# Kernel tuning notes

Hardware: AMD Instinct MI355X
Metric: run time of the kernel (lower is better)

The kernel has to match this reference:

```python
import jax, jax.numpy as jnp
import numpy as np

N_SIGMA = 2
N_CLASS = 8
FG_WEIGHT = jnp.array([10., 10., 10., 40., 80., 100., 60., 20.], dtype=jnp.float32)
W_INST, W_VAR, W_SEED = 1.0, 10.0, 1.0
MIN_PIXELS = 128


def lovasz_hinge_flat(logits, labels):
    # logits, labels: [P] flat; labels in {0,1}
    signs = 2.0 * labels - 1.0
    errors = 1.0 - logits * signs
    order = jnp.argsort(-errors)  # descending
    errors_sorted = errors[order]
    gt_sorted = labels[order]
    gts = gt_sorted.sum()
    inter = gts - jnp.cumsum(gt_sorted)
    union = gts + jnp.cumsum(1.0 - gt_sorted)
    jac = 1.0 - inter / union
    grad = jnp.concatenate([jac[:1], jac[1:] - jac[:-1]])
    return jnp.dot(jax.nn.relu(errors_sorted), jax.lax.stop_gradient(grad))


def setup_inputs() -> dict:
    key = jax.random.key(0)
    k1, k2, k3, k4 = jax.random.split(key, 4)
    B, H, W, N = 2, 512, 1024, 8
    prediction = jax.random.normal(k1, (B, 12, H, W), dtype=jnp.float32)
    bbox = jax.random.randint(k2, (B, 9, H, W), 0, 2, dtype=jnp.int32)
    masks = jax.random.randint(k3, (B, N, H, W), 0, 2, dtype=jnp.int32)
    cls_ids = jax.random.randint(k4, (B, N), 0, 8, dtype=jnp.int32)
    return {"prediction": prediction, "bbox": bbox, "masks": masks, "cls_ids": cls_ids}


def _forward(prediction, bbox, masks, cls_ids):
    B, C, H, W = prediction.shape
    N = masks.shape[1]
    sg = jax.lax.stop_gradient
    # coordinate map: full 2048/1024 linspace sliced to [:W]/[:H], as in the buffer
    xm = jnp.linspace(0.0, 2.0, 2048, dtype=prediction.dtype)[:W]
    ym = jnp.linspace(0.0, 1.0, 1024, dtype=prediction.dtype)[:H]
    xym = jnp.stack([jnp.broadcast_to(xm[None, :], (H, W)),
                     jnp.broadcast_to(ym[:, None], (H, W))], axis=0)  # [2,H,W]

    spatial_emb = jnp.tanh(prediction[:, 0:2]) + xym[None]            # [B,2,H,W]
    sigma = prediction[:, 2:2 + N_SIGMA]                               # [B,2,H,W]
    seed = jax.nn.sigmoid(prediction[:, 2 + N_SIGMA:2 + N_SIGMA + N_CLASS])  # [B,8,H,W]

    # background seed loss: sum over cls 1..8 of seed[cls-1]^2 where bbox[cls]==0
    bg = bbox[:, 1:9] == 0                                             # [B,8,H,W]
    seed_bg = jnp.sum(jnp.where(bg, seed * seed, 0.0), axis=(1, 2, 3))  # [B]

    m = (masks > 0).astype(prediction.dtype)                           # [B,N,H,W]
    cnt = m.sum(axis=(2, 3))                                           # [B,N]
    valid = (cnt >= MIN_PIXELS).astype(prediction.dtype)               # [B,N]
    cnt_safe = jnp.maximum(cnt, 1.0)

    # per-instance masked means (to_center=False -> center from spatial_emb)
    center = jnp.einsum('bnhw,bchw->bnc', m, spatial_emb) / cnt_safe[..., None]  # [B,N,2]
    s_mean = jnp.einsum('bnhw,bchw->bnc', m, sigma) / cnt_safe[..., None]        # [B,N,2]

    # var loss: mean over [n_sigma, P] of (sigma_in - s.detach())^2
    diff2 = (sigma[:, None] - sg(s_mean)[..., None, None]) ** 2        # [B,N,2,H,W]
    var_inst = jnp.einsum('bnchw,bnhw->bn', diff2, m) / (N_SIGMA * cnt_safe)

    s_exp = jnp.exp(s_mean * 10.0)                                     # [B,N,2]
    d2 = (spatial_emb[:, None] - center[..., None, None]) ** 2         # [B,N,2,H,W]
    dist = jnp.exp(-jnp.einsum('bnchw,bnc->bnhw', d2, s_exp))          # [B,N,H,W]

    # lovasz hinge per instance on dist*2-1 vs mask
    logits = (dist * 2.0 - 1.0).reshape(B * N, H * W)
    labels = m.reshape(B * N, H * W)
    lov = jax.vmap(lovasz_hinge_flat)(logits, labels).reshape(B, N)    # [B,N]

    # foreground seed loss
    seed_cls = jnp.take_along_axis(seed, cls_ids[..., None, None].astype(jnp.int32), axis=1)  # [B,N,H,W]
    fw = FG_WEIGHT[cls_ids]                                            # [B,N]
    seed_fg = fw * jnp.einsum('bnhw,bnhw->bn', m, (seed_cls - sg(dist)) ** 2)

    obj = valid.sum(axis=1)                                            # [B]
    obj_safe = jnp.maximum(obj, 1.0)
    inst_l = jnp.sum(lov * valid, axis=1) / obj_safe
    var_l = jnp.sum(var_inst * valid, axis=1) / obj_safe
    seed_l = (seed_bg + jnp.sum(seed_fg * valid, axis=1)) / (H * W)
    loss = jnp.mean(W_INST * inst_l + W_VAR * var_l + W_SEED * seed_l)
    return loss


def reference(prediction, bbox, masks, cls_ids):
    return _forward(prediction, bbox, masks, cls_ids)
```

## Files before the change

### kernel.cpp

```cpp
#include <hip/hip_runtime.h>
#include <cstdint>
#include <cstddef>

#define HW 524288
#define HW4 131072
#define NBIN 1024


__device__ __forceinline__ float wred(float v) {
#pragma unroll
  for (int o = 32; o > 0; o >>= 1) v += __shfl_xor(v, o, 64);
  return v;
}

__device__ __forceinline__ float fsig(float x) {
  return __builtin_amdgcn_rcpf(1.f + __expf(-x));
}
__device__ __forceinline__ float ftanh(float x) {
  return 1.f - 2.f * __builtin_amdgcn_rcpf(__expf(2.f * x) + 1.f);
}

__global__ __launch_bounds__(256) void pass1(
    const float* __restrict__ pred, const int* __restrict__ masks,
    double* __restrict__ acc)
{
  const int b = blockIdx.y;
  const int tid = threadIdx.x;
  const float4* pb4 = (const float4*)(pred + (size_t)b * 12 * HW);
  const int4*   mk4 = (const int4*)(masks + (size_t)b * 8 * HW);

  float c[8] = {0}, cx[8] = {0}, cy[8] = {0}, sx[8] = {0}, sy[8] = {0},
        sxx[8] = {0}, syy[8] = {0};

#pragma unroll
  for (int k = 0; k < 2; k++) {
    const int g = blockIdx.x * 512 + k * 256 + tid;
    int idx = g << 2;
    int h = idx >> 10, w = idx & 1023;
    float4 p0 = pb4[g];
    float4 p1 = pb4[HW4 + g];
    float4 s0 = pb4[2 * HW4 + g];
    float4 s1 = pb4[3 * HW4 + g];
    int4 mv[8];
#pragma unroll
    for (int n = 0; n < 8; n++) mv[n] = mk4[n * HW4 + g];

    float p0v[4] = {p0.x, p0.y, p0.z, p0.w}, p1v[4] = {p1.x, p1.y, p1.z, p1.w};
    float s0v[4] = {s0.x, s0.y, s0.z, s0.w}, s1v[4] = {s1.x, s1.y, s1.z, s1.w};
    float exv[4], eyv[4];
#pragma unroll
    for (int j = 0; j < 4; j++) {
      exv[j] = ftanh(p0v[j]) + (float)((w + j) * (2.0 / 2047.0));
      eyv[j] = ftanh(p1v[j]) + (float)(h * (1.0 / 1023.0));
    }
#pragma unroll
    for (int n = 0; n < 8; n++) {
      int mvv[4] = {mv[n].x, mv[n].y, mv[n].z, mv[n].w};
#pragma unroll
      for (int j = 0; j < 4; j++) {
        float mf = (mvv[j] > 0) ? 1.f : 0.f;
        c[n] += mf; cx[n] += mf * exv[j]; cy[n] += mf * eyv[j];
        sx[n] += mf * s0v[j]; sy[n] += mf * s1v[j];
        sxx[n] += mf * s0v[j] * s0v[j]; syy[n] += mf * s1v[j] * s1v[j];
      }
    }
  }

  __shared__ float red[4][56];
  int lane = tid & 63, wid = tid >> 6;
#pragma unroll
  for (int n = 0; n < 8; n++) {
    float r0 = wred(c[n]),  r1 = wred(cx[n]), r2 = wred(cy[n]),
          r3 = wred(sx[n]), r4 = wred(sy[n]), r5 = wred(sxx[n]),
          r6 = wred(syy[n]);
    if (lane == 0) {
      red[wid][n * 7 + 0] = r0; red[wid][n * 7 + 1] = r1;
      red[wid][n * 7 + 2] = r2; red[wid][n * 7 + 3] = r3;
      red[wid][n * 7 + 4] = r4; red[wid][n * 7 + 5] = r5;
      red[wid][n * 7 + 6] = r6;
    }
  }
  __syncthreads();
  if (tid < 56) {
    float s = red[0][tid] + red[1][tid] + red[2][tid] + red[3][tid];
    int n = tid / 7, q = tid % 7;
    atomicAdd(&acc[((size_t)b * 8 + n) * 8 + q], (double)s);
  }
}

__global__ __launch_bounds__(1024) void pass3(
    const float* __restrict__ pred, const int* __restrict__ bbox,
    const int* __restrict__ masks, const int* __restrict__ cls_ids,
    double* __restrict__ acc, double* __restrict__ seedbg,
    unsigned long long* __restrict__ ghist)
{
  const int seg = blockIdx.y;
  const int b = seg >> 3, n = seg & 7;
  const int tid = threadIdx.x;
  __shared__ unsigned hist[NBIN];
  __shared__ float redf[16][2];
  for (int j = tid; j < NBIN; j += 1024) hist[j] = 0;

  const double* a = acc + seg * 8;
  double cntd = a[0];
  double cs = cntd < 1.0 ? 1.0 : cntd;
  float cxv = (float)(a[1] / cs), cyv = (float)(a[2] / cs);
  float sex = __expf((float)(a[3] / cs) * 10.f);
  float sey = __expf((float)(a[4] / cs) * 10.f);
  int cls = cls_ids[b * 8 + n];
  const float4* pb4 = (const float4*)(pred + (size_t)b * 12 * HW);
  const float4* sp4 = pb4 + (size_t)(4 + cls) * HW4;
  const float4* sb4 = pb4 + (size_t)(4 + n) * HW4;
  const int4*   mp4 = (const int4*)(masks + (size_t)seg * HW);
  const int4*   bb4 = (const int4*)(bbox + (size_t)b * 9 * HW) + (1 + n) * HW4;
  __syncthreads();

  float sf = 0.f, sbg = 0.f;
  int gbase = blockIdx.x * 4096;
#pragma unroll
  for (int i = 0; i < 4; i++) {
    int g = gbase + i * 1024 + tid;
    int idx = g << 2;
    int h = idx >> 10, w = idx & 1023;
    float4 p0 = pb4[g];
    float4 p1 = pb4[HW4 + g];
    int4 mv = mp4[g];
    float4 sv = sp4[g];
    float4 sb = sb4[g];
    int4 bv = bb4[g];
    float p0v[4] = {p0.x, p0.y, p0.z, p0.w}, p1v[4] = {p1.x, p1.y, p1.z, p1.w};
    float svv[4] = {sv.x, sv.y, sv.z, sv.w}, sbv[4] = {sb.x, sb.y, sb.z, sb.w};
    int mvv[4] = {mv.x, mv.y, mv.z, mv.w}, bvv[4] = {bv.x, bv.y, bv.z, bv.w};
#pragma unroll
    for (int j = 0; j < 4; j++) {
      int m = (mvv[j] > 0) ? 1 : 0;
      float ex = ftanh(p0v[j]) + (float)((w + j) * (2.0 / 2047.0));
      float ey = ftanh(p1v[j]) + (float)(h * (1.0 / 1023.0));
      float dx = ex - cxv, dy = ey - cyv;
      float d = __expf(-(dx * dx * sex + dy * dy * sey));
      float df = fsig(svv[j]) - d;
      sf += m ? df * df : 0.f;
      float sgb = fsig(sbv[j]);
      sbg += (bvv[j] == 0) ? sgb * sgb : 0.f;
      float e = m ? 2.f - 2.f * d : 2.f * d;
      int k = (int)(e * 512.f); k = k > (NBIN - 1) ? (NBIN - 1) : k;
      atomicAdd(&hist[k], m ? 65536u : 1u);
    }
  }
  __syncthreads();

  unsigned long long* gh = ghist + (size_t)seg * NBIN;
  for (int j = tid; j < NBIN; j += 1024) {
    unsigned v = hist[j];
    if (v)
      atomicAdd(&gh[j], (unsigned long long)(v & 0xffffu) |
                        ((unsigned long long)(v >> 16) << 32));
  }

  float r0 = wred(sf), r1 = wred(sbg);
  int lane = tid & 63, wid = tid >> 6;
  if (lane == 0) { redf[wid][0] = r0; redf[wid][1] = r1; }
  __syncthreads();
  if (tid == 0) {
    float t = 0.f;
    for (int w2 = 0; w2 < 16; w2++) t += redf[w2][0];
    atomicAdd(&acc[seg * 8 + 7], (double)t);
  } else if (tid == 64) {
    float t = 0.f;
    for (int w2 = 0; w2 < 16; w2++) t += redf[w2][1];
    atomicAdd(&seedbg[b], (double)t);
  }
}

__global__ __launch_bounds__(256) void pass4(
    const unsigned long long* __restrict__ ghist, const double* __restrict__ acc,
    const double* __restrict__ seedbg, const int* __restrict__ cls_ids,
    float* __restrict__ lov, unsigned* __restrict__ ctr,
    float* __restrict__ out)
{
  const int seg = blockIdx.x;
  const int tid = threadIdx.x;
  const int lane = tid & 63, wid = tid >> 6;
  __shared__ __align__(16) unsigned lh[NBIN * 2];
  __shared__ unsigned wc[4], wp[4];
  __shared__ double sred[4];

  const uint4* gh4 = (const uint4*)(ghist + (size_t)seg * NBIN);
#pragma unroll
  for (int i = 0; i < 2; i++)
    ((uint4*)lh)[i * 256 + tid] = gh4[i * 256 + tid];
  __syncthreads();

  double G = acc[seg * 8 + 0];

  unsigned cntT = 0, posT = 0;
#pragma unroll
  for (int i = 0; i < 4; i++) {
    int kk = (NBIN - 1) - tid * 4 - i;
    unsigned h0 = lh[2 * kk], h1 = lh[2 * kk + 1];
    cntT += h0 + h1; posT += h1;
  }
  unsigned ic = cntT, ip = posT;
  for (int o = 1; o < 64; o <<= 1) {
    unsigned yc = __shfl_up(ic, o, 64), yp = __shfl_up(ip, o, 64);
    if (lane >= o) { ic += yc; ip += yp; }
  }
  if (lane == 63) { wc[wid] = ic; wp[wid] = ip; }
  __syncthreads();
  unsigned oc = 0, op = 0;
  for (int w2 = 0; w2 < wid; w2++) { oc += wc[w2]; op += wp[w2]; }
  unsigned p = oc + ic - cntT, C = op + ip - posT;

  double S = 0.0;
#pragma unroll
  for (int i = 0; i < 4; i++) {
    int kk = (NBIN - 1) - tid * 4 - i;
    unsigned n1 = lh[2 * kk + 1], n0 = lh[2 * kk];
    double ec = (kk + 0.5) * (1.0 / 512.0);
    if (n1) {
      S += (double)n1 * ec / (G + (double)(p - C));
      p += n1; C += n1;
    }
    if (n0) {
      double rem = G - (double)C;
      if (rem > 0.0) {
        double aa = G + (double)(p - C);
        S += ec * rem * (1.0 / aa - 1.0 / (aa + (double)n0));
      }
      p += n0;
    }
  }
#pragma unroll
  for (int o = 32; o > 0; o >>= 1) S += __shfl_xor(S, o, 64);
  if (lane == 0) sred[wid] = S;
  __syncthreads();

  if (tid == 0) {
    double St = sred[0] + sred[1] + sred[2] + sred[3];
    atomicExch(&lov[seg], (float)St);
    __threadfence();
    unsigned old = atomicAdd(ctr, 1u);
    if (old == 15u) {
      __threadfence();
      const float FG[8] = {10.f, 10.f, 10.f, 40.f, 80.f, 100.f, 60.f, 20.f};
      double total = 0.0;
      for (int b = 0; b < 2; b++) {
        double obj = 0, inst = 0, varl = 0, sfg = 0;
        for (int n = 0; n < 8; n++) {
          int s = b * 8 + n;
          const double* a = acc + s * 8;
          double cnt = a[0];
          double cs = cnt < 1.0 ? 1.0 : cnt;
          double smx = a[3] / cs, smy = a[4] / cs;
          double var = ((a[5] - cnt * smx * smx) + (a[6] - cnt * smy * smy)) /
                       (2.0 * cs);
          double v = (cnt >= 128.0) ? 1.0 : 0.0;
          double lv = (double)atomicAdd(&lov[s], 0.0f);
          obj += v;
          inst += lv * v;
          varl += var * v;
          sfg += (double)FG[cls_ids[s]] * a[7] * v;
        }
        double objs = obj < 1.0 ? 1.0 : obj;
        double seedl = (seedbg[b] + sfg) / (double)HW;
        total += inst / objs + 10.0 * (varl / objs) + seedl;
      }
      out[0] = (float)(0.5 * total);
    }
  }
}

extern "C" void kernel_launch(void* const* d_in, const int* in_sizes, int n_in,
                              void* d_out, int out_size, void* d_ws, size_t ws_size,
                              hipStream_t stream)
{
  (void)in_sizes; (void)n_in; (void)out_size; (void)ws_size;
  const float* pred  = (const float*)d_in[0];
  const int*   bbox  = (const int*)d_in[1];
  const int*   masks = (const int*)d_in[2];
  const int*   cls   = (const int*)d_in[3];

  char* ws = (char*)d_ws;
  double*             acc    = (double*)(ws + 0);
  double*             seedbg = (double*)(ws + 1024);
  float*              lov    = (float*)(ws + 1040);
  unsigned*           ctr    = (unsigned*)(ws + 1104);
  unsigned long long* ghist  = (unsigned long long*)(ws + 4096);

  hipMemsetAsync(d_ws, 0, 135168, stream);
  pass1<<<dim3(256, 2), 256, 0, stream>>>(pred, masks, acc);
  pass3<<<dim3(32, 16), 1024, 0, stream>>>(pred, bbox, masks, cls, acc, seedbg, ghist);
  pass4<<<16, 256, 0, stream>>>(ghist, acc, seedbg, cls, lov, ctr, (float*)d_out);
}
```

Baseline: 171.5 us.

## Fold final histogram reduction into pass3 and zero histogram inside pass1

Removes the separate pass4 kernel by having the last-finishing pass3 block compute all 16 Lovasz sums (one wavefront per segment) and the final loss. The large workspace memset is replaced by zeroing the histogram buffer inside pass1, leaving only a tiny memset. This cuts launch and memset overhead, at the cost of a serialized tail in one block and a changed launch-bounds occupancy hint.

```diff
diff --git a/kernel.cpp b/kernel.cpp
--- a/kernel.cpp
+++ b/kernel.cpp
@@ -22,10 +22,14 @@
 
 __global__ __launch_bounds__(256) void pass1(
     const float* __restrict__ pred, const int* __restrict__ masks,
-    double* __restrict__ acc)
+    double* __restrict__ acc, unsigned* __restrict__ ghz)
 {
   const int b = blockIdx.y;
   const int tid = threadIdx.x;
+  {
+    int blk = blockIdx.y * 256 + blockIdx.x;
+    if (tid < 64) ghz[blk * 64 + tid] = 0;
+  }
   const float4* pb4 = (const float4*)(pred + (size_t)b * 12 * HW);
   const int4*   mk4 = (const int4*)(masks + (size_t)b * 8 * HW);
 
@@ -88,25 +92,28 @@
   }
 }
 
-__global__ __launch_bounds__(1024) void pass3(
+__global__ __launch_bounds__(1024, 8) void pass3(
     const float* __restrict__ pred, const int* __restrict__ bbox,
     const int* __restrict__ masks, const int* __restrict__ cls_ids,
     double* __restrict__ acc, double* __restrict__ seedbg,
-    unsigned long long* __restrict__ ghist)
+    unsigned long long* __restrict__ ghist, unsigned* __restrict__ ctr,
+    float* __restrict__ out)
 {
   const int seg = blockIdx.y;
   const int b = seg >> 3, n = seg & 7;
   const int tid = threadIdx.x;
   __shared__ unsigned hist[NBIN];
   __shared__ float redf[16][2];
+  __shared__ float lovs[16];
+  __shared__ int isLast;
   for (int j = tid; j < NBIN; j += 1024) hist[j] = 0;
 
   const double* a = acc + seg * 8;
   double cntd = a[0];
-  double cs = cntd < 1.0 ? 1.0 : cntd;
-  float cxv = (float)(a[1] / cs), cyv = (float)(a[2] / cs);
-  float sex = __expf((float)(a[3] / cs) * 10.f);
-  float sey = __expf((float)(a[4] / cs) * 10.f);
+  double cs0 = cntd < 1.0 ? 1.0 : cntd;
+  float cxv = (float)(a[1] / cs0), cyv = (float)(a[2] / cs0);
+  float sex = __expf((float)(a[3] / cs0) * 10.f);
+  float sey = __expf((float)(a[4] / cs0) * 10.f);
   int cls = cls_ids[b * 8 + n];
   const float4* pb4 = (const float4*)(pred + (size_t)b * 12 * HW);
   const float4* sp4 = pb4 + (size_t)(4 + cls) * HW4;
@@ -170,103 +177,98 @@
     for (int w2 = 0; w2 < 16; w2++) t += redf[w2][1];
     atomicAdd(&seedbg[b], (double)t);
   }
-}
-
-__global__ __launch_bounds__(256) void pass4(
-    const unsigned long long* __restrict__ ghist, const double* __restrict__ acc,
-    const double* __restrict__ seedbg, const int* __restrict__ cls_ids,
-    float* __restrict__ lov, unsigned* __restrict__ ctr,
-    float* __restrict__ out)
-{
-  const int seg = blockIdx.x;
-  const int tid = threadIdx.x;
-  const int lane = tid & 63, wid = tid >> 6;
-  __shared__ __align__(16) unsigned lh[NBIN * 2];
-  __shared__ unsigned wc[4], wp[4];
-  __shared__ double sred[4];
-
-  const uint4* gh4 = (const uint4*)(ghist + (size_t)seg * NBIN);
-#pragma unroll
-  for (int i = 0; i < 2; i++)
-    ((uint4*)lh)[i * 256 + tid] = gh4[i * 256 + tid];
-  __syncthreads();
-
-  double G = acc[seg * 8 + 0];
-
-  unsigned cntT = 0, posT = 0;
-#pragma unroll
-  for (int i = 0; i < 4; i++) {
-    int kk = (NBIN - 1) - tid * 4 - i;
-    unsigned h0 = lh[2 * kk], h1 = lh[2 * kk + 1];
-    cntT += h0 + h1; posT += h1;
-  }
-  unsigned ic = cntT, ip = posT;
-  for (int o = 1; o < 64; o <<= 1) {
-    unsigned yc = __shfl_up(ic, o, 64), yp = __shfl_up(ip, o, 64);
-    if (lane >= o) { ic += yc; ip += yp; }
-  }
-  if (lane == 63) { wc[wid] = ic; wp[wid] = ip; }
-  __syncthreads();
-  unsigned oc = 0, op = 0;
-  for (int w2 = 0; w2 < wid; w2++) { oc += wc[w2]; op += wp[w2]; }
-  unsigned p = oc + ic - cntT, C = op + ip - posT;
-
-  double S = 0.0;
-#pragma unroll
-  for (int i = 0; i < 4; i++) {
-    int kk = (NBIN - 1) - tid * 4 - i;
-    unsigned n1 = lh[2 * kk + 1], n0 = lh[2 * kk];
-    double ec = (kk + 0.5) * (1.0 / 512.0);
-    if (n1) {
-      S += (double)n1 * ec / (G + (double)(p - C));
-      p += n1; C += n1;
-    }
-    if (n0) {
-      double rem = G - (double)C;
-      if (rem > 0.0) {
-        double aa = G + (double)(p - C);
-        S += ec * rem * (1.0 / aa - 1.0 / (aa + (double)n0));
-      }
-      p += n0;
-    }
-  }
-#pragma unroll
-  for (int o = 32; o > 0; o >>= 1) S += __shfl_xor(S, o, 64);
-  if (lane == 0) sred[wid] = S;
-  __syncthreads();
-
+  __syncthreads();
   if (tid == 0) {
-    double St = sred[0] + sred[1] + sred[2] + sred[3];
-    atomicExch(&lov[seg], (float)St);
     __threadfence();
     unsigned old = atomicAdd(ctr, 1u);
-    if (old == 15u) {
-      __threadfence();
-      const float FG[8] = {10.f, 10.f, 10.f, 40.f, 80.f, 100.f, 60.f, 20.f};
-      double total = 0.0;
-      for (int b = 0; b < 2; b++) {
-        double obj = 0, inst = 0, varl = 0, sfg = 0;
-        for (int n = 0; n < 8; n++) {
-          int s = b * 8 + n;
-          const double* a = acc + s * 8;
-          double cnt = a[0];
-          double cs = cnt < 1.0 ? 1.0 : cnt;
-          double smx = a[3] / cs, smy = a[4] / cs;
-          double var = ((a[5] - cnt * smx * smx) + (a[6] - cnt * smy * smy)) /
-                       (2.0 * cs);
-          double v = (cnt >= 128.0) ? 1.0 : 0.0;
-          double lv = (double)atomicAdd(&lov[s], 0.0f);
-          obj += v;
-          inst += lv * v;
-          varl += var * v;
-          sfg += (double)FG[cls_ids[s]] * a[7] * v;
+    isLast = (old == 16 * 32 - 1) ? 1 : 0;
+  }
+  __syncthreads();
+  if (!isLast) return;
+  __threadfence();
+
+  {
+    int s2 = wid;
+    const unsigned long long* gh2 = ghist + (size_t)s2 * NBIN;
+    double G = __hip_atomic_load(&acc[s2 * 8 + 0], __ATOMIC_RELAXED,
+                                 __HIP_MEMORY_SCOPE_AGENT);
+    unsigned cntT = 0, posT = 0;
+    unsigned long long hv[16];
+#pragma unroll
+    for (int i = 0; i < 16; i++) {
+      int kk = (NBIN - 1) - lane * 16 - i;
+      hv[i] = __hip_atomic_load(&gh2[kk], __ATOMIC_RELAXED,
+                                __HIP_MEMORY_SCOPE_AGENT);
+      unsigned h0 = (unsigned)hv[i], h1 = (unsigned)(hv[i] >> 32);
+      cntT += h0 + h1; posT += h1;
+    }
+    unsigned ic = cntT, ip = posT;
+    for (int o = 1; o < 64; o <<= 1) {
+      unsigned yc = __shfl_up(ic, o, 64), yp = __shfl_up(ip, o, 64);
+      if (lane >= o) { ic += yc; ip += yp; }
+    }
+    unsigned p = ic - cntT, C = ip - posT;
+    double S = 0.0;
+#pragma unroll
+    for (int i = 0; i < 16; i++) {
+      int kk = (NBIN - 1) - lane * 16 - i;
+      unsigned n0c = (unsigned)hv[i], n1c = (unsigned)(hv[i] >> 32);
+      double ec = (kk + 0.5) * (1.0 / 512.0);
+      if (n1c) {
+        S += (double)n1c * ec / (G + (double)(p - C));
+        p += n1c; C += n1c;
+      }
+      if (n0c) {
+        double rem = G - (double)C;
+        if (rem > 0.0) {
+          double aa = G + (double)(p - C);
+          S += ec * rem * (1.0 / aa - 1.0 / (aa + (double)n0c));
         }
-        double objs = obj < 1.0 ? 1.0 : obj;
-        double seedl = (seedbg[b] + sfg) / (double)HW;
-        total += inst / objs + 10.0 * (varl / objs) + seedl;
-      }
-      out[0] = (float)(0.5 * total);
-    }
+        p += n0c;
+      }
+    }
+#pragma unroll
+    for (int o = 32; o > 0; o >>= 1) S += __shfl_xor(S, o, 64);
+    if (lane == 0) lovs[s2] = (float)S;
+  }
+  __syncthreads();
+
+  if (tid == 0) {
+    const float FG[8] = {10.f, 10.f, 10.f, 40.f, 80.f, 100.f, 60.f, 20.f};
+    double total = 0.0;
+    for (int bb = 0; bb < 2; bb++) {
+      double obj = 0, inst = 0, varl = 0, sfg = 0;
+      for (int nn = 0; nn < 8; nn++) {
+        int s = bb * 8 + nn;
+        double cnt = __hip_atomic_load(&acc[s * 8 + 0], __ATOMIC_RELAXED,
+                                       __HIP_MEMORY_SCOPE_AGENT);
+        double a3 = __hip_atomic_load(&acc[s * 8 + 3], __ATOMIC_RELAXED,
+                                      __HIP_MEMORY_SCOPE_AGENT);
+        double a4 = __hip_atomic_load(&acc[s * 8 + 4], __ATOMIC_RELAXED,
+                                      __HIP_MEMORY_SCOPE_AGENT);
+        double a5 = __hip_atomic_load(&acc[s * 8 + 5], __ATOMIC_RELAXED,
+                                      __HIP_MEMORY_SCOPE_AGENT);
+        double a6 = __hip_atomic_load(&acc[s * 8 + 6], __ATOMIC_RELAXED,
+                                      __HIP_MEMORY_SCOPE_AGENT);
+        double a7 = __hip_atomic_load(&acc[s * 8 + 7], __ATOMIC_RELAXED,
+                                      __HIP_MEMORY_SCOPE_AGENT);
+        double cs = cnt < 1.0 ? 1.0 : cnt;
+        double smx = a3 / cs, smy = a4 / cs;
+        double var = ((a5 - cnt * smx * smx) + (a6 - cnt * smy * smy)) /
+                     (2.0 * cs);
+        double v = (cnt >= 128.0) ? 1.0 : 0.0;
+        obj += v;
+        inst += (double)lovs[s] * v;
+        varl += var * v;
+        sfg += (double)FG[cls_ids[s]] * a7 * v;
+      }
+      double objs = obj < 1.0 ? 1.0 : obj;
+      double sb2 = __hip_atomic_load(&seedbg[bb], __ATOMIC_RELAXED,
+                                     __HIP_MEMORY_SCOPE_AGENT);
+      double seedl = (sb2 + sfg) / (double)HW;
+      total += inst / objs + 10.0 * (varl / objs) + seedl;
+    }
+    out[0] = (float)(0.5 * total);
   }
 }
 
@@ -283,12 +285,11 @@
   char* ws = (char*)d_ws;
   double*             acc    = (double*)(ws + 0);
   double*             seedbg = (double*)(ws + 1024);
-  float*              lov    = (float*)(ws + 1040);
   unsigned*           ctr    = (unsigned*)(ws + 1104);
   unsigned long long* ghist  = (unsigned long long*)(ws + 4096);
 
-  hipMemsetAsync(d_ws, 0, 135168, stream);
-  pass1<<<dim3(256, 2), 256, 0, stream>>>(pred, masks, acc);
-  pass3<<<dim3(32, 16), 1024, 0, stream>>>(pred, bbox, masks, cls, acc, seedbg, ghist);
-  pass4<<<16, 256, 0, stream>>>(ghist, acc, seedbg, cls, lov, ctr, (float*)d_out);
-}
+  hipMemsetAsync(d_ws, 0, 1152, stream);
+  pass1<<<dim3(256, 2), 256, 0, stream>>>(pred, masks, acc, (unsigned*)ghist);
+  pass3<<<dim3(32, 16), 1024, 0, stream>>>(pred, bbox, masks, cls, acc, seedbg,
+                                           ghist, ctr, (float*)d_out);
+}
```

Result: slower. 205.6 us (+19.9%).
